# Performance work log

Hardware: AMD Instinct MI355X
Metric: run time of the kernel (lower is better)

## Reference

```python
import jax, jax.numpy as jnp
import numpy as np

NEG_INF = -1e20  # the repo defines INF = 1e20
TOPK = 10


def setup_inputs() -> dict:
    key = jax.random.key(0)
    k1, k2 = jax.random.split(key)
    B, N, D, H = 8, 2048, 512, 512
    context = jax.random.normal(k1, (B, N, D), dtype=jnp.float32)
    ctx_mask = jnp.ones((B, N), dtype=jnp.int32)  # all positions valid
    W = jax.random.normal(k2, (H, D), dtype=jnp.float32) * 0.02  # linear_sim weight
    return {"context": context, "W": W, "ctx_mask": ctx_mask}


def reference(context, W, ctx_mask):
    # context_fc = relu(linear_sim(context))        : [B, N, H]
    ctx_fc = jax.nn.relu(jnp.einsum('bnd,hd->bnh', context, W))
    # attention = context_fc @ context_fc^T         : [B, N, N]
    att = jnp.einsum('bnh,bmh->bnm', ctx_fc, ctx_fc)
    # masked_fill where ctx_mask == 0 (both row and column)
    m = ctx_mask.astype(bool)
    att = jnp.where(m[:, None, :], att, NEG_INF)
    att = jnp.where(m[:, :, None], att, NEG_INF)
    # build_knn_neighbourhood: keep top-k per row, everything else -INF
    k = min(TOPK, att.shape[-1])
    knn_val, knn_ind = jax.lax.top_k(att, k)  # [B, N, k]
    B, N, _ = att.shape
    bi = jnp.arange(B)[:, None, None]
    ri = jnp.arange(N)[None, :, None]
    adj = jnp.full(att.shape, NEG_INF, dtype=att.dtype).at[bi, ri, knn_ind].set(knn_val)
    return adj
```

## Files before the change

### kernel.cpp

```cpp
#include <hip/hip_runtime.h>
#include <hip/hip_bf16.h>

#define NEG_INF -1e20f

typedef __bf16 bf16x8 __attribute__((ext_vector_type(8)));
typedef float  f32x4  __attribute__((ext_vector_type(4)));

__device__ inline unsigned short f2bf(float x) {
    unsigned u = __float_as_uint(x);
    unsigned r = u + 0x7fffu + ((u >> 16) & 1u);
    return (unsigned short)(r >> 16);
}
__device__ inline float bf2f(unsigned short h) {
    return __uint_as_float((unsigned)h << 16);
}
__device__ inline unsigned fkey(float f) {
    unsigned u = __float_as_uint(f);
    return (u & 0x80000000u) ? ~u : (u | 0x80000000u);
}

__global__ __launch_bounds__(256) void split3_all(
        const float* __restrict__ ctx, const float* __restrict__ W,
        unsigned short* __restrict__ C1, unsigned short* __restrict__ C2,
        unsigned short* __restrict__ C3, unsigned short* __restrict__ W1,
        unsigned short* __restrict__ W2, unsigned short* __restrict__ W3) {
    const int b = blockIdx.x;
    const int t = threadIdx.x;
    const float* src;
    unsigned short *p1, *p2, *p3;
    int base;
    if (b < 2048) { src = ctx; p1 = C1; p2 = C2; p3 = C3; base = b * 1024; }
    else          { src = W;   p1 = W1; p2 = W2; p3 = W3; base = (b - 2048) * 1024; }
#pragma unroll
    for (int it = 0; it < 4; ++it) {
        int i = base + it * 256 + t;
        float4 v = ((const float4*)src)[i];
        ushort4 a, bb, c;
        float r;
        a.x = f2bf(v.x); r = v.x - bf2f(a.x); bb.x = f2bf(r); c.x = f2bf(r - bf2f(bb.x));
        a.y = f2bf(v.y); r = v.y - bf2f(a.y); bb.y = f2bf(r); c.y = f2bf(r - bf2f(bb.y));
        a.z = f2bf(v.z); r = v.z - bf2f(a.z); bb.z = f2bf(r); c.z = f2bf(r - bf2f(bb.z));
        a.w = f2bf(v.w); r = v.w - bf2f(a.w); bb.w = f2bf(r); c.w = f2bf(r - bf2f(bb.w));
        ((ushort4*)p1)[i] = a;
        ((ushort4*)p2)[i] = bb;
        ((ushort4*)p3)[i] = c;
    }
}

__global__ __launch_bounds__(256, 2) void fc_mfma6(
        const unsigned short* __restrict__ A1, const unsigned short* __restrict__ A2,
        const unsigned short* __restrict__ A3, const unsigned short* __restrict__ B1,
        const unsigned short* __restrict__ B2, const unsigned short* __restrict__ B3,
        unsigned short* __restrict__ Fhi, unsigned short* __restrict__ Flo) {
    __shared__ char lds[49152];

    const int t     = threadIdx.x;
    const int mBase = blockIdx.x * 128;
    const int hBase = blockIdx.y * 128;
    const int w = t >> 6, lane = t & 63;
    const int q = lane >> 4, ln = lane & 15;
    const int wn = (w >> 1) * 64;
    const int wm = (w & 1) * 64;

    f32x4 acc[4][4] = {};

    for (int kt = 0; kt < 512; kt += 32) {
#pragma unroll
        for (int p = 0; p < 3; ++p) {
            const unsigned short* pl = (p == 0) ? A1 : (p == 1) ? A2 : A3;
#pragma unroll
            for (int rr = 0; rr < 2; ++rr) {
                int chunk = rr * 256 + t;
                int row   = chunk >> 2;
                int c     = (chunk & 3) ^ ((row >> 1) & 3);
                const unsigned short* g = pl + ((size_t)(mBase + row) * 512 + kt + c * 8);
                char* l = lds + p * 8192 + chunk * 16;
                __builtin_amdgcn_global_load_lds(
                    (const __attribute__((address_space(1))) void*)g,
                    (__attribute__((address_space(3))) void*)l, 16, 0, 0);
            }
        }
#pragma unroll
        for (int p = 0; p < 3; ++p) {
            const unsigned short* pl = (p == 0) ? B1 : (p == 1) ? B2 : B3;
#pragma unroll
            for (int rr = 0; rr < 2; ++rr) {
                int chunk = rr * 256 + t;
                int row   = chunk >> 2;
                int c     = (chunk & 3) ^ ((row >> 1) & 3);
                const unsigned short* g = pl + ((size_t)(hBase + row) * 512 + kt + c * 8);
                char* l = lds + 24576 + p * 8192 + chunk * 16;
                __builtin_amdgcn_global_load_lds(
                    (const __attribute__((address_space(1))) void*)g,
                    (__attribute__((address_space(3))) void*)l, 16, 0, 0);
            }
        }
        __syncthreads();

        bf16x8 a1[4], a2[4], a3[4], b1[4], b2[4], b3[4];
#pragma unroll
        for (int i = 0; i < 4; ++i) {
            int mA = wn + i * 16 + ln;
            int oA = (mA * 4 + (q ^ ((mA >> 1) & 3))) * 16;
            a1[i] = *(const bf16x8*)(lds +     0 + oA);
            a2[i] = *(const bf16x8*)(lds +  8192 + oA);
            a3[i] = *(const bf16x8*)(lds + 16384 + oA);
            int mB = wm + i * 16 + ln;
            int oB = (mB * 4 + (q ^ ((mB >> 1) & 3))) * 16;
            b1[i] = *(const bf16x8*)(lds + 24576 + oB);
            b2[i] = *(const bf16x8*)(lds + 32768 + oB);
            b3[i] = *(const bf16x8*)(lds + 40960 + oB);
        }
#pragma unroll
        for (int i = 0; i < 4; ++i)
#pragma unroll
            for (int j = 0; j < 4; ++j) {
                acc[i][j] = __builtin_amdgcn_mfma_f32_16x16x32_bf16(a1[i], b1[j], acc[i][j], 0, 0, 0);
                acc[i][j] = __builtin_amdgcn_mfma_f32_16x16x32_bf16(a1[i], b2[j], acc[i][j], 0, 0, 0);
                acc[i][j] = __builtin_amdgcn_mfma_f32_16x16x32_bf16(a2[i], b1[j], acc[i][j], 0, 0, 0);
                acc[i][j] = __builtin_amdgcn_mfma_f32_16x16x32_bf16(a2[i], b2[j], acc[i][j], 0, 0, 0);
                acc[i][j] = __builtin_amdgcn_mfma_f32_16x16x32_bf16(a1[i], b3[j], acc[i][j], 0, 0, 0);
                acc[i][j] = __builtin_amdgcn_mfma_f32_16x16x32_bf16(a3[i], b1[j], acc[i][j], 0, 0, 0);
            }
        __syncthreads();
    }

    unsigned* tb = (unsigned*)(lds + w * 4352);
    const int rg = lane >> 4;
    const int c4 = lane & 15;
#pragma unroll
    for (int i = 0; i < 4; ++i) {
#pragma unroll
        for (int j = 0; j < 4; ++j)
#pragma unroll
            for (int r = 0; r < 4; ++r) {
                float v = fmaxf(acc[i][j][r], 0.f);
                unsigned short hi = f2bf(v);
                unsigned short lo = f2bf(v - bf2f(hi));
                tb[(q * 4 + r) * 68 + j * 16 + ln] =
                    (unsigned)hi | ((unsigned)lo << 16);
            }
#pragma unroll
        for (int it = 0; it < 4; ++it) {
            int row = it * 4 + rg;
            uint4 pk = *(const uint4*)&tb[row * 68 + c4 * 4];
            ushort4 h, l;
            h.x = (unsigned short)pk.x; l.x = (unsigned short)(pk.x >> 16);
            h.y = (unsigned short)pk.y; l.y = (unsigned short)(pk.y >> 16);
            h.z = (unsigned short)pk.z; l.z = (unsigned short)(pk.z >> 16);
            h.w = (unsigned short)pk.w; l.w = (unsigned short)(pk.w >> 16);
            size_t off = (size_t)(mBase + wn + i * 16 + row) * 512 + hBase + wm + c4 * 4;
            *(ushort4*)(Fhi + off) = h;
            *(ushort4*)(Flo + off) = l;
        }
    }
}

__global__ __launch_bounds__(256, 2) void att_mfma_sym(
        const unsigned short* __restrict__ Fhi, const unsigned short* __restrict__ Flo,
        const int* __restrict__ mask, float* __restrict__ out) {
    __shared__ char lds[32768];

    const int t = threadIdx.x;
    const int b = blockIdx.x & 7;
    int p = blockIdx.x >> 3, ti = 0;
    while (p >= 16 - ti) { p -= 16 - ti; ++ti; }
    const int tj = ti + p;
    const int nBase = ti * 128;
    const int mBase = tj * 128;
    const int w    = t >> 6, lane = t & 63;
    const int q    = lane >> 4, ln = lane & 15;
    const int wn   = (w >> 1) * 64;
    const int wm   = (w & 1) * 64;
    const size_t rowB = (size_t)b * 2048;

    f32x4 acc[4][4] = {};

    for (int kt = 0; kt < 512; kt += 32) {
#pragma unroll
        for (int pp = 0; pp < 4; ++pp) {
            const unsigned short* plane = (pp & 1) ? Flo : Fhi;
            int rbase = (pp < 2) ? nBase : mBase;
#pragma unroll
            for (int r = 0; r < 2; ++r) {
                int chunk = r * 256 + t;
                int row   = chunk >> 2;
                int c     = (chunk & 3) ^ ((row >> 1) & 3);
                const unsigned short* g =
                    plane + ((rowB + rbase + row) * 512 + kt + c * 8);
                char* l = lds + pp * 8192 + chunk * 16;
                __builtin_amdgcn_global_load_lds(
                    (const __attribute__((address_space(1))) void*)g,
                    (__attribute__((address_space(3))) void*)l, 16, 0, 0);
            }
        }
        __syncthreads();

        bf16x8 ah[4], al[4], bh[4], bl[4];
#pragma unroll
        for (int i = 0; i < 4; ++i) {
            int mA = wn + i * 16 + ln;
            int oA = (mA * 4 + (q ^ ((mA >> 1) & 3))) * 16;
            ah[i] = *(const bf16x8*)(lds +     0 + oA);
            al[i] = *(const bf16x8*)(lds +  8192 + oA);
            int mB = wm + i * 16 + ln;
            int oB = (mB * 4 + (q ^ ((mB >> 1) & 3))) * 16;
            bh[i] = *(const bf16x8*)(lds + 16384 + oB);
            bl[i] = *(const bf16x8*)(lds + 24576 + oB);
        }
#pragma unroll
        for (int i = 0; i < 4; ++i)
#pragma unroll
            for (int j = 0; j < 4; ++j) {
                acc[i][j] = __builtin_amdgcn_mfma_f32_16x16x32_bf16(ah[i], bh[j], acc[i][j], 0, 0, 0);
                acc[i][j] = __builtin_amdgcn_mfma_f32_16x16x32_bf16(ah[i], bl[j], acc[i][j], 0, 0, 0);
                acc[i][j] = __builtin_amdgcn_mfma_f32_16x16x32_bf16(al[i], bh[j], acc[i][j], 0, 0, 0);
            }
        __syncthreads();
    }

    const int* mb = mask + b * 2048;
    float* outB = out + (size_t)b * 2048 * 2048;
    int cm[4];
#pragma unroll
    for (int j = 0; j < 4; ++j) cm[j] = mb[mBase + wm + j * 16 + ln];

    float* tb = (float*)(lds + w * 4352);
    const int rg = lane >> 4;
    const int c4 = lane & 15;
    const bool mirror = (ti != tj);
#pragma unroll
    for (int i = 0; i < 4; ++i) {
        int n0 = nBase + wn + i * 16;
        int rmv[4];
#pragma unroll
        for (int r = 0; r < 4; ++r) rmv[r] = mb[n0 + q * 4 + r];
#pragma unroll
        for (int j = 0; j < 4; ++j)
#pragma unroll
            for (int r = 0; r < 4; ++r) {
                float v = ((rmv[r] != 0) & (cm[j] != 0)) ? acc[i][j][r] : NEG_INF;
                tb[(q * 4 + r) * 68 + j * 16 + ln] = v;
            }
#pragma unroll
        for (int it = 0; it < 4; ++it) {
            int row = it * 4 + rg;
            float4 vv = *(const float4*)&tb[row * 68 + c4 * 4];
            *(float4*)(outB + (size_t)(n0 + row) * 2048 + mBase + wm + c4 * 4) = vv;
        }
        if (mirror) {
#pragma unroll
            for (int ps = 0; ps < 4; ++ps) {
                float4 mv;
                mv.x = tb[(ps * 4 + 0) * 68 + lane];
                mv.y = tb[(ps * 4 + 1) * 68 + lane];
                mv.z = tb[(ps * 4 + 2) * 68 + lane];
                mv.w = tb[(ps * 4 + 3) * 68 + lane];
                *(float4*)(outB + (size_t)(mBase + wm + lane) * 2048 + n0 + ps * 4) = mv;
            }
        }
    }
}

__global__ __launch_bounds__(256) void topk_rows(float* __restrict__ att) {
    __shared__ float patch[4][2048];

    const int t    = threadIdx.x;
    const int w    = t >> 6;
    const int lane = t & 63;
    float* row = att + ((size_t)blockIdx.x * 4 + w) * 2048;

    unsigned key[32];
#pragma unroll
    for (int s = 0; s < 8; ++s) {
        float4 v = *(const float4*)(row + lane * 32 + s * 4);
        key[s * 4 + 0] = fkey(v.x);
        key[s * 4 + 1] = fkey(v.y);
        key[s * 4 + 2] = fkey(v.z);
        key[s * 4 + 3] = fkey(v.w);
    }

    unsigned h1 = key[0]; int i1 = 0;
#pragma unroll
    for (int j = 1; j < 32; ++j)
        if (key[j] > h1) { h1 = key[j]; i1 = j; }
    unsigned h2 = 0; int i2 = 0;
#pragma unroll
    for (int j = 0; j < 32; ++j) {
        bool ok = (j != i1) && (key[j] > h2);
        h2 = ok ? key[j] : h2;
        i2 = ok ? j : i2;
    }
    bool h2valid = true;
    unsigned taken = 0;

    unsigned myk = 0; int myidx = 0;
    for (int r = 0; r < 10; ++r) {
        unsigned M = h1;
#pragma unroll
        for (int off = 1; off < 64; off <<= 1) {
            unsigned o = __shfl_xor(M, off, 64);
            M = (o > M) ? o : M;
        }
        unsigned long long ball = __ballot(h1 == M);
        int src  = __ffsll(ball) - 1;
        int wloc = __shfl(i1, src, 64);
        if (lane == r) { myk = M; myidx = src * 32 + wloc; }
        if (lane == src) {
            taken |= 1u << i1;
            if (h2valid) { h1 = h2; i1 = i2; h2valid = false; }
            else {
                unsigned bh = 0; int bi = 0;
#pragma unroll
                for (int j = 0; j < 32; ++j) {
                    bool ok = (((taken >> j) & 1u) == 0u) && (key[j] > bh);
                    bh = ok ? key[j] : bh;
                    bi = ok ? j : bi;
                }
                h1 = bh; i1 = bi;
            }
        }
    }

    float* pw = patch[w];
    float4 ninf4 = make_float4(NEG_INF, NEG_INF, NEG_INF, NEG_INF);
#pragma unroll
    for (int s = 0; s < 8; ++s) ((float4*)pw)[s * 64 + lane] = ninf4;
    if (lane < 10) {
        unsigned fu = (myk & 0x80000000u) ? (myk ^ 0x80000000u) : ~myk;
        pw[myidx] = __uint_as_float(fu);
    }
#pragma unroll
    for (int s = 0; s < 8; ++s)
        ((float4*)row)[s * 64 + lane] = ((float4*)pw)[s * 64 + lane];
}

extern "C" void kernel_launch(void* const* d_in, const int* in_sizes, int n_in,
                              void* d_out, int out_size, void* d_ws, size_t ws_size,
                              hipStream_t stream) {
    const float* ctx  = (const float*)d_in[0];
    const float* W    = (const float*)d_in[1];
    const int*   mask = (const int*)d_in[2];
    float* out = (float*)d_out;

    const size_t CN = (size_t)16384 * 512;
    const size_t WN = (size_t)512 * 512;
    unsigned short* C1 = (unsigned short*)d_out;
    unsigned short* C2 = C1 + CN;
    unsigned short* C3 = C2 + CN;
    unsigned short* W1 = C3 + CN;
    unsigned short* W2 = W1 + WN;
    unsigned short* W3 = W2 + WN;

    unsigned short* Fhi = (unsigned short*)d_ws;
    unsigned short* Flo = Fhi + CN;

    dim3 blk(256);
    split3_all<<<dim3(2112), blk, 0, stream>>>(ctx, W, C1, C2, C3, W1, W2, W3);
    fc_mfma6<<<dim3(128, 4), blk, 0, stream>>>(C1, C2, C3, W1, W2, W3, Fhi, Flo);
    att_mfma_sym<<<dim3(1088), blk, 0, stream>>>(Fhi, Flo, mask, out);
    topk_rows<<<dim3(4096), blk, 0, stream>>>(out);
}
```

Baseline: 305.0 us.

## Fuse per-tile top-10 candidate selection into attention GEMM epilogue

The attention kernel no longer writes the full B×N×N score matrix. Each 128×128 tile's epilogue selects per-row top-10 candidates, including the mirrored transpose for off-diagonal tiles, and writes them to a compact candidate buffer. A new merge kernel reduces the 16 tiles × 10 candidates per row to the final top-10 and writes the output row. This removes a full write and re-read of the 128MB score matrix, at the cost of extra LDS syncs and selection work inside the GEMM kernel.

After: 356.2 us. 1.17x slower.

```diff
diff --git a/kernel.cpp b/kernel.cpp
--- a/kernel.cpp
+++ b/kernel.cpp
@@ -17,6 +17,10 @@
 __device__ inline unsigned fkey(float f) {
     unsigned u = __float_as_uint(f);
     return (u & 0x80000000u) ? ~u : (u | 0x80000000u);
+}
+__device__ inline float unfkey(unsigned k) {
+    unsigned fu = (k & 0x80000000u) ? (k ^ 0x80000000u) : ~k;
+    return __uint_as_float(fu);
 }
 
 __global__ __launch_bounds__(256) void split3_all(
@@ -156,9 +160,55 @@
     }
 }
 
-__global__ __launch_bounds__(256, 2) void att_mfma_sym(
+__device__ __forceinline__ void select10(const float* prow, int g,
+        unsigned& c0k, int& c0c, unsigned& c1k, int& c1c) {
+    unsigned k[16];
+#pragma unroll
+    for (int s = 0; s < 4; ++s) {
+        float4 v = *(const float4*)(prow + s * 4);
+        k[s*4+0] = fkey(v.x); k[s*4+1] = fkey(v.y);
+        k[s*4+2] = fkey(v.z); k[s*4+3] = fkey(v.w);
+    }
+    unsigned h1 = k[0]; int i1 = 0;
+#pragma unroll
+    for (int j = 1; j < 16; ++j) if (k[j] > h1) { h1 = k[j]; i1 = j; }
+    unsigned h2 = 0; int i2 = 0;
+#pragma unroll
+    for (int j = 0; j < 16; ++j) { bool ok = (j != i1) && (k[j] > h2); h2 = ok ? k[j] : h2; i2 = ok ? j : i2; }
+    bool h2v = true; unsigned taken = 0;
+    c0k = 0; c0c = 0; c1k = 0; c1c = 0;
+#pragma unroll
+    for (int r = 0; r < 10; ++r) {
+        unsigned long long P = ((unsigned long long)h1 << 32) | (unsigned)(g * 16 + i1);
+#pragma unroll
+        for (int off = 1; off < 8; off <<= 1) {
+            unsigned long long Q = __shfl_xor(P, off, 64);
+            P = (Q > P) ? Q : P;
+        }
+        unsigned M = (unsigned)(P >> 32);
+        int cl = (int)(P & 0xffffu);
+        if (r < 8) { if (g == r)     { c0k = M; c0c = cl; } }
+        else       { if (g == r - 8) { c1k = M; c1c = cl; } }
+        if ((cl >> 4) == g) {
+            taken |= 1u << (cl & 15);
+            if (h2v) { h1 = h2; i1 = i2; h2v = false; }
+            else {
+                unsigned bh = 0; int bi = 0;
+#pragma unroll
+                for (int jx = 0; jx < 16; ++jx) {
+                    bool ok = (((taken >> jx) & 1u) == 0u) && (k[jx] > bh);
+                    bh = ok ? k[jx] : bh; bi = ok ? jx : bi;
+                }
+                h1 = bh; i1 = bi;
+            }
+        }
+    }
+}
+
+__global__ __launch_bounds__(256, 2) void att_cand(
         const unsigned short* __restrict__ Fhi, const unsigned short* __restrict__ Flo,
-        const int* __restrict__ mask, float* __restrict__ out) {
+        const int* __restrict__ mask, float* __restrict__ cvO,
+        unsigned short* __restrict__ ciO) {
     __shared__ char lds[32768];
 
     const int t = threadIdx.x;
@@ -219,82 +269,103 @@
         __syncthreads();
     }
 
+    float* patch = (float*)lds;
     const int* mb = mask + b * 2048;
-    float* outB = out + (size_t)b * 2048 * 2048;
-    int cm[4];
-#pragma unroll
-    for (int j = 0; j < 4; ++j) cm[j] = mb[mBase + wm + j * 16 + ln];
-
-    float* tb = (float*)(lds + w * 4352);
-    const int rg = lane >> 4;
-    const int c4 = lane & 15;
-    const bool mirror = (ti != tj);
+
+    int cmj[4];
+#pragma unroll
+    for (int j = 0; j < 4; ++j) cmj[j] = mb[mBase + wm + j * 16 + ln];
+    int rmAll[4][4];
+#pragma unroll
+    for (int i = 0; i < 4; ++i)
+#pragma unroll
+        for (int r = 0; r < 4; ++r) rmAll[i][r] = mb[nBase + wn + i * 16 + q * 4 + r];
+
+    const int pr = t >> 3, g = t & 7;
+
 #pragma unroll
     for (int i = 0; i < 4; ++i) {
-        int n0 = nBase + wn + i * 16;
-        int rmv[4];
-#pragma unroll
-        for (int r = 0; r < 4; ++r) rmv[r] = mb[n0 + q * 4 + r];
+        int prBase = (w >> 1) * 16;
 #pragma unroll
         for (int j = 0; j < 4; ++j)
 #pragma unroll
             for (int r = 0; r < 4; ++r) {
-                float v = ((rmv[r] != 0) & (cm[j] != 0)) ? acc[i][j][r] : NEG_INF;
-                tb[(q * 4 + r) * 68 + j * 16 + ln] = v;
-            }
-#pragma unroll
-        for (int it = 0; it < 4; ++it) {
-            int row = it * 4 + rg;
-            float4 vv = *(const float4*)&tb[row * 68 + c4 * 4];
-            *(float4*)(outB + (size_t)(n0 + row) * 2048 + mBase + wm + c4 * 4) = vv;
-        }
-        if (mirror) {
-#pragma unroll
-            for (int ps = 0; ps < 4; ++ps) {
-                float4 mv;
-                mv.x = tb[(ps * 4 + 0) * 68 + lane];
-                mv.y = tb[(ps * 4 + 1) * 68 + lane];
-                mv.z = tb[(ps * 4 + 2) * 68 + lane];
-                mv.w = tb[(ps * 4 + 3) * 68 + lane];
-                *(float4*)(outB + (size_t)(mBase + wm + lane) * 2048 + n0 + ps * 4) = mv;
-            }
-        }
-    }
-}
-
-__global__ __launch_bounds__(256) void topk_rows(float* __restrict__ att) {
+                float v = ((rmAll[i][r] != 0) & (cmj[j] != 0)) ? acc[i][j][r] : NEG_INF;
+                patch[(prBase + q * 4 + r) * 132 + wm + j * 16 + ln] = v;
+            }
+        __syncthreads();
+        {
+            unsigned c0k, c1k; int c0c, c1c;
+            select10(patch + pr * 132 + g * 16, g, c0k, c0c, c1k, c1c);
+            int rowG = nBase + ((pr >> 4) << 6) + i * 16 + (pr & 15);
+            size_t cb = (((size_t)b * 2048 + rowG) * 16 + tj) * 10;
+            cvO[cb + g] = unfkey(c0k);
+            ciO[cb + g] = (unsigned short)(mBase + c0c);
+            if (g < 2) {
+                cvO[cb + 8 + g] = unfkey(c1k);
+                ciO[cb + 8 + g] = (unsigned short)(nBase == mBase ? mBase + c1c : mBase + c1c);
+            }
+        }
+        __syncthreads();
+    }
+
+    if (ti != tj) {
+#pragma unroll
+        for (int c2 = 0; c2 < 4; ++c2) {
+            if ((w & 1) == (c2 >> 1)) {
+                int jb = (c2 & 1) * 2;
+#pragma unroll
+                for (int jj = 0; jj < 2; ++jj) {
+                    int j = jb + jj;
+#pragma unroll
+                    for (int i2 = 0; i2 < 4; ++i2)
+#pragma unroll
+                        for (int r = 0; r < 4; ++r) {
+                            float v = ((rmAll[i2][r] != 0) & (cmj[j] != 0)) ? acc[i2][j][r] : NEG_INF;
+                            patch[(jj * 16 + ln) * 132 + wn + i2 * 16 + q * 4 + r] = v;
+                        }
+                }
+            }
+            __syncthreads();
+            {
+                unsigned c0k, c1k; int c0c, c1c;
+                select10(patch + pr * 132 + g * 16, g, c0k, c0c, c1k, c1c);
+                int rowG = mBase + c2 * 32 + pr;
+                size_t cb = (((size_t)b * 2048 + rowG) * 16 + ti) * 10;
+                cvO[cb + g] = unfkey(c0k);
+                ciO[cb + g] = (unsigned short)(nBase + c0c);
+                if (g < 2) {
+                    cvO[cb + 8 + g] = unfkey(c1k);
+                    ciO[cb + 8 + g] = (unsigned short)(nBase + c1c);
+                }
+            }
+            __syncthreads();
+        }
+    }
+}
+
+__global__ __launch_bounds__(256) void topk_merge(
+        const float* __restrict__ cv, const unsigned short* __restrict__ ci,
+        float* __restrict__ out) {
     __shared__ float patch[4][2048];
 
-    const int t    = threadIdx.x;
-    const int w    = t >> 6;
-    const int lane = t & 63;
-    float* row = att + ((size_t)blockIdx.x * 4 + w) * 2048;
-
-    unsigned key[32];
-#pragma unroll
-    for (int s = 0; s < 8; ++s) {
-        float4 v = *(const float4*)(row + lane * 32 + s * 4);
-        key[s * 4 + 0] = fkey(v.x);
-        key[s * 4 + 1] = fkey(v.y);
-        key[s * 4 + 2] = fkey(v.z);
-        key[s * 4 + 3] = fkey(v.w);
-    }
-
-    unsigned h1 = key[0]; int i1 = 0;
-#pragma unroll
-    for (int j = 1; j < 32; ++j)
-        if (key[j] > h1) { h1 = key[j]; i1 = j; }
-    unsigned h2 = 0; int i2 = 0;
-#pragma unroll
-    for (int j = 0; j < 32; ++j) {
-        bool ok = (j != i1) && (key[j] > h2);
-        h2 = ok ? key[j] : h2;
-        i2 = ok ? j : i2;
-    }
-    bool h2valid = true;
+    const int t = threadIdx.x, w = t >> 6, lane = t & 63;
+    const size_t R = (size_t)blockIdx.x * 4 + w;
+    const float* v = cv + R * 160;
+    const unsigned short* id = ci + R * 160;
+
+    float v0 = v[lane], v1 = v[lane + 64];
+    int   c0 = id[lane], c1 = id[lane + 64];
+    float v2 = NEG_INF;  int c2 = 0;
+    if (lane < 32) { v2 = v[lane + 128]; c2 = id[lane + 128]; }
+    unsigned k0 = fkey(v0), k1 = fkey(v1), k2 = fkey(v2);
+
+    unsigned h1 = k0; int i1 = 0;
+    if (k1 > h1) { h1 = k1; i1 = 1; }
+    if (k2 > h1) { h1 = k2; i1 = 2; }
     unsigned taken = 0;
-
-    unsigned myk = 0; int myidx = 0;
+    unsigned myk = 0; int mycol = 0;
+
     for (int r = 0; r < 10; ++r) {
         unsigned M = h1;
 #pragma unroll
@@ -303,22 +374,17 @@
             M = (o > M) ? o : M;
         }
         unsigned long long ball = __ballot(h1 == M);
-        int src  = __ffsll(ball) - 1;
-        int wloc = __shfl(i1, src, 64);
-        if (lane == r) { myk = M; myidx = src * 32 + wloc; }
+        int src = __ffsll(ball) - 1;
+        int csel = (i1 == 0) ? c0 : ((i1 == 1) ? c1 : c2);
+        int wcol = __shfl(csel, src, 64);
+        if (lane == r) { myk = M; mycol = wcol; }
         if (lane == src) {
             taken |= 1u << i1;
-            if (h2valid) { h1 = h2; i1 = i2; h2valid = false; }
-            else {
-                unsigned bh = 0; int bi = 0;
-#pragma unroll
-                for (int j = 0; j < 32; ++j) {
-                    bool ok = (((taken >> j) & 1u) == 0u) && (key[j] > bh);
-                    bh = ok ? key[j] : bh;
-                    bi = ok ? j : bi;
-                }
-                h1 = bh; i1 = bi;
-            }
+            unsigned bh = 0; int bi = 0;
+            if (!(taken & 1u))            { bh = k0; bi = 0; }
+            if (!(taken & 2u) && k1 > bh) { bh = k1; bi = 1; }
+            if (!(taken & 4u) && k2 > bh) { bh = k2; bi = 2; }
+            h1 = bh; i1 = bi;
         }
     }
 
@@ -326,10 +392,8 @@
     float4 ninf4 = make_float4(NEG_INF, NEG_INF, NEG_INF, NEG_INF);
 #pragma unroll
     for (int s = 0; s < 8; ++s) ((float4*)pw)[s * 64 + lane] = ninf4;
-    if (lane < 10) {
-        unsigned fu = (myk & 0x80000000u) ? (myk ^ 0x80000000u) : ~myk;
-        pw[myidx] = __uint_as_float(fu);
-    }
+    if (lane < 10) pw[mycol] = unfkey(myk);
+    float* row = out + R * 2048;
 #pragma unroll
     for (int s = 0; s < 8; ++s)
         ((float4*)row)[s * 64 + lane] = ((float4*)pw)[s * 64 + lane];
@@ -351,13 +415,15 @@
     unsigned short* W1 = C3 + CN;
     unsigned short* W2 = W1 + WN;
     unsigned short* W3 = W2 + WN;
-
-    unsigned short* Fhi = (unsigned short*)d_ws;
+    unsigned short* Fhi = W3 + WN;
     unsigned short* Flo = Fhi + CN;
+
+    float* cv          = (float*)d_ws;
+    unsigned short* ci = (unsigned short*)(cv + (size_t)8 * 2048 * 160);
 
     dim3 blk(256);
     split3_all<<<dim3(2112), blk, 0, stream>>>(ctx, W, C1, C2, C3, W1, W2, W3);
     fc_mfma6<<<dim3(128, 4), blk, 0, stream>>>(C1, C2, C3, W1, W2, W3, Fhi, Flo);
-    att_mfma_sym<<<dim3(1088), blk, 0, stream>>>(Fhi, Flo, mask, out);
-    topk_rows<<<dim3(4096), blk, 0, stream>>>(out);
-}
+    att_cand<<<dim3(1088), blk, 0, stream>>>(Fhi, Flo, mask, cv, ci);
+    topk_merge<<<dim3(4096), blk, 0, stream>>>(cv, ci, out);
+}
```

## Emit per-chunk row maxima in attention kernel and filter top-k candidates

Applied to the files above, without the earlier changes.

The attention GEMM epilogue now writes, for each row, the maximum of every 64-column chunk (including the mirrored transpose tiles) to a small workspace array. The top-k kernel takes the 10th-largest chunk max as a lower bound, reloads only the chunks that can hold top-10 values, and ranks the surviving candidates. It falls back to the old full-row selection when more than 64 survive. Launch bounds rise to 3 waves per SIMD, which adds register pressure and extra shuffles in the epilogue in exchange for less selection work per row.

After: 296.0 us, median of 2. 1.03x faster.

```diff
diff --git a/kernel.cpp b/kernel.cpp
--- a/kernel.cpp
+++ b/kernel.cpp
@@ -17,6 +17,10 @@
 __device__ inline unsigned fkey(float f) {
     unsigned u = __float_as_uint(f);
     return (u & 0x80000000u) ? ~u : (u | 0x80000000u);
+}
+__device__ inline float unfkey(unsigned k) {
+    unsigned fu = (k & 0x80000000u) ? (k ^ 0x80000000u) : ~k;
+    return __uint_as_float(fu);
 }
 
 __global__ __launch_bounds__(256) void split3_all(
@@ -156,9 +160,10 @@
     }
 }
 
-__global__ __launch_bounds__(256, 2) void att_mfma_sym(
+__global__ __launch_bounds__(256, 3) void att_sym_cand(
         const unsigned short* __restrict__ Fhi, const unsigned short* __restrict__ Flo,
-        const int* __restrict__ mask, float* __restrict__ out) {
+        const int* __restrict__ mask, float* __restrict__ out,
+        float* __restrict__ cv2) {
     __shared__ char lds[32768];
 
     const int t = threadIdx.x;
@@ -221,9 +226,14 @@
 
     const int* mb = mask + b * 2048;
     float* outB = out + (size_t)b * 2048 * 2048;
-    int cm[4];
-#pragma unroll
-    for (int j = 0; j < 4; ++j) cm[j] = mb[mBase + wm + j * 16 + ln];
+    int cmj[4];
+#pragma unroll
+    for (int j = 0; j < 4; ++j) cmj[j] = mb[mBase + wm + j * 16 + ln];
+    int rmAll[4][4];
+#pragma unroll
+    for (int i = 0; i < 4; ++i)
+#pragma unroll
+        for (int r = 0; r < 4; ++r) rmAll[i][r] = mb[nBase + wn + i * 16 + q * 4 + r];
 
     float* tb = (float*)(lds + w * 4352);
     const int rg = lane >> 4;
@@ -232,14 +242,26 @@
 #pragma unroll
     for (int i = 0; i < 4; ++i) {
         int n0 = nBase + wn + i * 16;
-        int rmv[4];
-#pragma unroll
-        for (int r = 0; r < 4; ++r) rmv[r] = mb[n0 + q * 4 + r];
+#pragma unroll
+        for (int r = 0; r < 4; ++r) {
+            float m4 = NEG_INF;
+#pragma unroll
+            for (int j = 0; j < 4; ++j) {
+                float v = ((rmAll[i][r] != 0) & (cmj[j] != 0)) ? acc[i][j][r] : NEG_INF;
+                m4 = fmaxf(m4, v);
+            }
+            m4 = fmaxf(m4, __shfl_xor(m4, 1, 64));
+            m4 = fmaxf(m4, __shfl_xor(m4, 2, 64));
+            m4 = fmaxf(m4, __shfl_xor(m4, 4, 64));
+            m4 = fmaxf(m4, __shfl_xor(m4, 8, 64));
+            if (ln == 0)
+                cv2[(rowB + n0 + q * 4 + r) * 32 + tj * 2 + (w & 1)] = m4;
+        }
 #pragma unroll
         for (int j = 0; j < 4; ++j)
 #pragma unroll
             for (int r = 0; r < 4; ++r) {
-                float v = ((rmv[r] != 0) & (cm[j] != 0)) ? acc[i][j][r] : NEG_INF;
+                float v = ((rmAll[i][r] != 0) & (cmj[j] != 0)) ? acc[i][j][r] : NEG_INF;
                 tb[(q * 4 + r) * 68 + j * 16 + ln] = v;
             }
 #pragma unroll
@@ -260,76 +282,146 @@
             }
         }
     }
-}
-
-__global__ __launch_bounds__(256) void topk_rows(float* __restrict__ att) {
-    __shared__ float patch[4][2048];
-
-    const int t    = threadIdx.x;
-    const int w    = t >> 6;
-    const int lane = t & 63;
-    float* row = att + ((size_t)blockIdx.x * 4 + w) * 2048;
-
-    unsigned key[32];
+    if (mirror) {
+#pragma unroll
+        for (int j = 0; j < 4; ++j) {
+            float m16 = NEG_INF;
+#pragma unroll
+            for (int i2 = 0; i2 < 4; ++i2)
+#pragma unroll
+                for (int r = 0; r < 4; ++r) {
+                    float v = ((rmAll[i2][r] != 0) & (cmj[j] != 0)) ? acc[i2][j][r] : NEG_INF;
+                    m16 = fmaxf(m16, v);
+                }
+            m16 = fmaxf(m16, __shfl_xor(m16, 16, 64));
+            m16 = fmaxf(m16, __shfl_xor(m16, 32, 64));
+            if (q == 0)
+                cv2[(rowB + mBase + wm + j * 16 + ln) * 32 + ti * 2 + (w >> 1)] = m16;
+        }
+    }
+}
+
+__global__ __launch_bounds__(256) void topk_filter(
+        const float* __restrict__ cv2, float* __restrict__ att) {
+    __shared__ float  patch[4][2048];
+    __shared__ float2 surv[4][64];
+
+    const int t = threadIdx.x, w = t >> 6, lane = t & 63;
+    const size_t R = (size_t)blockIdx.x * 4 + w;
+    float* row = att + R * 2048;
+
+    float cnd = (lane < 32) ? cv2[R * 32 + lane] : NEG_INF;
+    int rk = 0;
+#pragma unroll
+    for (int j = 0; j < 32; ++j) {
+        float vj = __shfl(cnd, j, 64);
+        rk += ((vj > cnd) || (vj == cnd && j < lane)) ? 1 : 0;
+    }
+    unsigned long long bl = __ballot((lane < 32) && (rk == 9));
+    float L = __shfl(cnd, __ffsll(bl) - 1, 64);
+    unsigned long long hsel = __ballot((lane < 32) && (cnd >= L));
+    int hFirst = __ffsll(hsel) - 1;
+
+    const bool sel = (hsel >> (lane >> 1)) & 1ull;
+    const float* src = row + (sel ? lane * 32 : hFirst * 64 + (lane & 1) * 32);
+    float4 v4[8];
+#pragma unroll
+    for (int s = 0; s < 8; ++s) v4[s] = *(const float4*)(src + s * 4);
+
+    int nsurv = 0;
+    const unsigned long long lmask = (1ull << lane) - 1;
+    auto push = [&](float val, int col) {
+        bool pr = sel && (val >= L);
+        unsigned long long pb = __ballot(pr);
+        if (pr) {
+            int idx = nsurv + (int)__popcll(pb & lmask);
+            if (idx < 64) surv[w][idx] = make_float2(val, __int_as_float(col));
+        }
+        nsurv += (int)__popcll(pb);
+    };
 #pragma unroll
     for (int s = 0; s < 8; ++s) {
-        float4 v = *(const float4*)(row + lane * 32 + s * 4);
-        key[s * 4 + 0] = fkey(v.x);
-        key[s * 4 + 1] = fkey(v.y);
-        key[s * 4 + 2] = fkey(v.z);
-        key[s * 4 + 3] = fkey(v.w);
-    }
-
-    unsigned h1 = key[0]; int i1 = 0;
-#pragma unroll
-    for (int j = 1; j < 32; ++j)
-        if (key[j] > h1) { h1 = key[j]; i1 = j; }
-    unsigned h2 = 0; int i2 = 0;
-#pragma unroll
-    for (int j = 0; j < 32; ++j) {
-        bool ok = (j != i1) && (key[j] > h2);
-        h2 = ok ? key[j] : h2;
-        i2 = ok ? j : i2;
-    }
-    bool h2valid = true;
-    unsigned taken = 0;
-
-    unsigned myk = 0; int myidx = 0;
-    for (int r = 0; r < 10; ++r) {
-        unsigned M = h1;
-#pragma unroll
-        for (int off = 1; off < 64; off <<= 1) {
-            unsigned o = __shfl_xor(M, off, 64);
-            M = (o > M) ? o : M;
-        }
-        unsigned long long ball = __ballot(h1 == M);
-        int src  = __ffsll(ball) - 1;
-        int wloc = __shfl(i1, src, 64);
-        if (lane == r) { myk = M; myidx = src * 32 + wloc; }
-        if (lane == src) {
-            taken |= 1u << i1;
-            if (h2valid) { h1 = h2; i1 = i2; h2valid = false; }
-            else {
-                unsigned bh = 0; int bi = 0;
-#pragma unroll
-                for (int j = 0; j < 32; ++j) {
-                    bool ok = (((taken >> j) & 1u) == 0u) && (key[j] > bh);
-                    bh = ok ? key[j] : bh;
-                    bi = ok ? j : bi;
+        int cb = lane * 32 + s * 4;
+        push(v4[s].x, cb + 0);
+        push(v4[s].y, cb + 1);
+        push(v4[s].z, cb + 2);
+        push(v4[s].w, cb + 3);
+    }
+
+    bool win = false; float myv = NEG_INF; int mycol = 0;
+    if (nsurv <= 64) {
+        float sv = NEG_INF; int sc = 0x7fffffff;
+        if (lane < nsurv) {
+            float2 s2 = surv[w][lane];
+            sv = s2.x; sc = __float_as_int(s2.y);
+        }
+        int r2 = 0;
+        for (int j = 0; j < nsurv; ++j) {
+            float2 sj = surv[w][j];
+            int cj = __float_as_int(sj.y);
+            r2 += ((sj.x > sv) || (sj.x == sv && cj < sc)) ? 1 : 0;
+        }
+        win = (lane < nsurv) && (r2 < 10);
+        myv = sv; mycol = win ? sc : 0;
+    } else {
+        unsigned key[32];
+#pragma unroll
+        for (int s = 0; s < 8; ++s) {
+            float4 v = *(const float4*)(row + lane * 32 + s * 4);
+            key[s * 4 + 0] = fkey(v.x);
+            key[s * 4 + 1] = fkey(v.y);
+            key[s * 4 + 2] = fkey(v.z);
+            key[s * 4 + 3] = fkey(v.w);
+        }
+        unsigned h1 = key[0]; int i1 = 0;
+#pragma unroll
+        for (int j = 1; j < 32; ++j)
+            if (key[j] > h1) { h1 = key[j]; i1 = j; }
+        unsigned h2 = 0; int i2 = 0;
+#pragma unroll
+        for (int j = 0; j < 32; ++j) {
+            bool ok = (j != i1) && (key[j] > h2);
+            h2 = ok ? key[j] : h2;
+            i2 = ok ? j : i2;
+        }
+        bool h2valid = true;
+        unsigned taken = 0;
+        unsigned myk = 0; int myidx = 0;
+        for (int r = 0; r < 10; ++r) {
+            unsigned M = h1;
+#pragma unroll
+            for (int off = 1; off < 64; off <<= 1) {
+                unsigned o = __shfl_xor(M, off, 64);
+                M = (o > M) ? o : M;
+            }
+            unsigned long long ball = __ballot(h1 == M);
+            int srcb = __ffsll(ball) - 1;
+            int wloc = __shfl(i1, srcb, 64);
+            if (lane == r) { myk = M; myidx = srcb * 32 + wloc; }
+            if (lane == srcb) {
+                taken |= 1u << i1;
+                if (h2valid) { h1 = h2; i1 = i2; h2valid = false; }
+                else {
+                    unsigned bh = 0; int bi = 0;
+#pragma unroll
+                    for (int j = 0; j < 32; ++j) {
+                        bool ok = (((taken >> j) & 1u) == 0u) && (key[j] > bh);
+                        bh = ok ? key[j] : bh;
+                        bi = ok ? j : bi;
+                    }
+                    h1 = bh; i1 = bi;
                 }
-                h1 = bh; i1 = bi;
-            }
-        }
+            }
+        }
+        win = (lane < 10);
+        myv = unfkey(myk); mycol = win ? myidx : 0;
     }
 
     float* pw = patch[w];
     float4 ninf4 = make_float4(NEG_INF, NEG_INF, NEG_INF, NEG_INF);
 #pragma unroll
     for (int s = 0; s < 8; ++s) ((float4*)pw)[s * 64 + lane] = ninf4;
-    if (lane < 10) {
-        unsigned fu = (myk & 0x80000000u) ? (myk ^ 0x80000000u) : ~myk;
-        pw[myidx] = __uint_as_float(fu);
-    }
+    if (win) pw[mycol] = myv;
 #pragma unroll
     for (int s = 0; s < 8; ++s)
         ((float4*)row)[s * 64 + lane] = ((float4*)pw)[s * 64 + lane];
@@ -352,12 +444,13 @@
     unsigned short* W2 = W1 + WN;
     unsigned short* W3 = W2 + WN;
 
-    unsigned short* Fhi = (unsigned short*)d_ws;
+    float* cv2 = (float*)d_ws;
+    unsigned short* Fhi = (unsigned short*)(cv2 + (size_t)16384 * 32);
     unsigned short* Flo = Fhi + CN;
 
     dim3 blk(256);
     split3_all<<<dim3(2112), blk, 0, stream>>>(ctx, W, C1, C2, C3, W1, W2, W3);
     fc_mfma6<<<dim3(128, 4), blk, 0, stream>>>(C1, C2, C3, W1, W2, W3, Fhi, Flo);
-    att_mfma_sym<<<dim3(1088), blk, 0, stream>>>(Fhi, Flo, mask, out);
-    topk_rows<<<dim3(4096), blk, 0, stream>>>(out);
-}
+    att_sym_cand<<<dim3(1088), blk, 0, stream>>>(Fhi, Flo, mask, out, cv2);
+    topk_filter<<<dim3(4096), blk, 0, stream>>>(cv2, out);
+}
```
